# Kernel optimization log

Measured on AMD Instinct MI355X. Metric: run time of the kernel, lower is better.

Reference implementation:

```python
import jax, jax.numpy as jnp
import numpy as np

K = 20
EPS = 1e-5  # BatchNorm eps
SLOPE = 0.2  # LeakyReLU negative slope


def _lrelu(y):
    return jnp.where(y > 0, y, SLOPE * y)


def _knn_idx(x):
    # x: [B, C, N] -> idx [B, N, K] of nearest neighbors (largest of negative sq dist)
    inner = -2.0 * jnp.einsum('bcn,bcm->bnm', x, x)
    xx = jnp.sum(x * x, axis=1)  # [B, N]
    pd = -xx[:, :, None] - inner - xx[:, None, :]  # [B, N, N]
    return jax.lax.top_k(pd, K)[1]


def _graph_feature(x):
    # x: [B, C, N] -> [B, 2C, N, K] = cat(neighbor - center, center)
    idx = _knn_idx(x)
    xt = jnp.transpose(x, (0, 2, 1))  # [B, N, C]
    nb = jax.vmap(lambda f, i: f[i])(xt, idx)  # [B, N, K, C]
    ctr = xt[:, :, None, :]
    feat = jnp.concatenate([nb - ctr, jnp.broadcast_to(ctr, nb.shape)], axis=-1)
    return jnp.transpose(feat, (0, 3, 1, 2))


def _bn(y, p, ch_axis):
    g, b, m, v = p[0], p[1], p[2], p[3]
    shape = [1] * y.ndim
    shape[ch_axis] = -1
    scale = (g / jnp.sqrt(v + EPS)).reshape(shape)
    return (y - m.reshape(shape)) * scale + b.reshape(shape)


def _conv_block(x, w, bn):
    f = _graph_feature(x)  # [B, 2C_in, N, K]
    y = jnp.einsum('bcnk,oc->bonk', f, w)  # 1x1 conv, no bias
    y = _lrelu(_bn(y, bn, 1))
    return jnp.max(y, axis=-1)  # max over K neighbors -> [B, C_out, N]


def setup_inputs() -> dict:
    key = jax.random.key(0)
    ks = jax.random.split(key, 20)
    B, N = 8, 1024
    inp = {
        'x': jax.random.normal(ks[0], (B, 3, N), jnp.float32),
        'w0': jax.random.normal(ks[1], (64, 6), jnp.float32) * 0.1,
        'w1': jax.random.normal(ks[2], (64, 128), jnp.float32) * 0.1,
        'w2': jax.random.normal(ks[3], (128, 128), jnp.float32) * 0.1,
        'w3': jax.random.normal(ks[4], (256, 256), jnp.float32) * 0.1,
        'bn0': jax.random.uniform(ks[5], (4, 64), jnp.float32) + 0.1,
        'bn1': jax.random.uniform(ks[6], (4, 64), jnp.float32) + 0.1,
        'bn2': jax.random.uniform(ks[7], (4, 128), jnp.float32) + 0.1,
        'bn3': jax.random.uniform(ks[8], (4, 256), jnp.float32) + 0.1,
        'we': jax.random.normal(ks[9], (1024, 512), jnp.float32) * 0.05,
        'bne': jax.random.uniform(ks[10], (4, 1024), jnp.float32) + 0.1,
        'wf0': jax.random.normal(ks[11], (512, 2048), jnp.float32) * 0.02,
        'bnf0': jax.random.uniform(ks[12], (4, 512), jnp.float32) + 0.1,
        'wf1': jax.random.normal(ks[13], (256, 512), jnp.float32) * 0.05,
        'bnf1': jax.random.uniform(ks[14], (4, 256), jnp.float32) + 0.1,
        'wfin': jax.random.normal(ks[15], (64, 256), jnp.float32) * 0.05,
        'bfin': jax.random.normal(ks[16], (64,), jnp.float32) * 0.05,
    }
    return inp


def reference(x, w0, w1, w2, w3, bn0, bn1, bn2, bn3, we, bne, wf0, bnf0, wf1, bnf1, wfin, bfin):
    B = x.shape[0]
    x1 = _conv_block(x, w0, bn0)   # [B, 64, N]
    x2 = _conv_block(x1, w1, bn1)  # [B, 64, N]
    x3 = _conv_block(x2, w2, bn2)  # [B, 128, N]
    x4 = _conv_block(x3, w3, bn3)  # [B, 256, N]
    cat = jnp.concatenate([x1, x2, x3, x4], axis=1)  # [B, 512, N]
    e = _lrelu(_bn(jnp.einsum('bcn,oc->bon', cat, we), bne, 1))  # [B, 1024, N]
    p1 = jnp.max(e, axis=-1)
    p2 = jnp.mean(e, axis=-1)
    h = jnp.concatenate([p1, p2], axis=1)  # [B, 2048]
    h = _lrelu(_bn(h @ wf0.T, bnf0, 1))  # [B, 512]; dropout is eval-mode identity
    h = _lrelu(_bn(h @ wf1.T, bnf1, 1))  # [B, 256]
    return h @ wfin.T + bfin  # [B, 64]
```

## Files before the change

kernel.cpp:

```cpp
#include <hip/hip_runtime.h>
#include <math.h>

#define N_PTS 1024
#define BATCH 8
#define KNN 20
#define EPSB 1e-5f
#define SLOPE 0.2f

typedef __attribute__((ext_vector_type(8))) short short8;
typedef __attribute__((ext_vector_type(4))) float f32x4;
typedef unsigned short ushort_t;
typedef unsigned long long u64;

__device__ __forceinline__ float lrelu(float y) { return y > 0.f ? y : SLOPE * y; }

__device__ __forceinline__ ushort_t f2bf(float f) {
    union { float f; unsigned u; } v; v.f = f;
    unsigned r = v.u + 0x7FFF + ((v.u >> 16) & 1);
    return (ushort_t)(r >> 16);
}

__device__ __forceinline__ void wprep_one(const float* __restrict__ w, float* __restrict__ wpt,
                                          int C, int Cout, int g) {
    int M2 = 2 * Cout;
    if (g >= C * M2) return;
    int c = g / M2, m = g - c * M2;
    float v;
    if (m < Cout) v = w[(size_t)m * 2 * C + c];
    else { int o = m - Cout; v = w[(size_t)o * 2 * C + C + c] - w[(size_t)o * 2 * C + c]; }
    wpt[(size_t)c * M2 + m] = v;
}

__global__ void prep_kernel(const float* __restrict__ we, ushort_t* __restrict__ weh,
                            const float* __restrict__ w0, float* __restrict__ wpt0,
                            const float* __restrict__ w1, float* __restrict__ wpt1,
                            const float* __restrict__ w2, float* __restrict__ wpt2,
                            const float* __restrict__ w3, float* __restrict__ wpt3) {
    int bx = blockIdx.x, tid = threadIdx.x;
    if (bx < 512) {
        int g = bx * 256 + tid;
        float4 v = ((const float4*)we)[g];
        ushort4 o;
        o.x = f2bf(v.x); o.y = f2bf(v.y); o.z = f2bf(v.z); o.w = f2bf(v.w);
        ((ushort4*)weh)[g] = o;
    } else if (bx < 514) {
        wprep_one(w0, wpt0, 3, 64, (bx - 512) * 256 + tid);
    } else if (bx < 546) {
        wprep_one(w1, wpt1, 64, 64, (bx - 514) * 256 + tid);
    } else if (bx < 610) {
        wprep_one(w2, wpt2, 64, 128, (bx - 546) * 256 + tid);
    } else {
        wprep_one(w3, wpt3, 128, 256, (bx - 610) * 256 + tid);
    }
}

__global__ void __launch_bounds__(64)
xx_kernel(const float* __restrict__ x, float* __restrict__ xx, int C, int bstride) {
    int b = blockIdx.y;
    int n = blockIdx.x * 64 + threadIdx.x;
    const float* xb = x + (size_t)b * bstride + n;
    float s = 0.f;
    #pragma unroll 4
    for (int c = 0; c < C; c++) { float v = xb[(size_t)c * N_PTS]; s += v * v; }
    xx[b * N_PTS + n] = s;
}

__global__ void __launch_bounds__(256)
pdabv_kernel(const float* __restrict__ x, const float* __restrict__ wpt,
             const float* __restrict__ xx,
             float* __restrict__ pd, float* __restrict__ A, float* __restrict__ Bv,
             int C, int Cout, int bstride, int pdTiles) {
    int b = blockIdx.z;
    int nt = blockIdx.y;
    int bx = blockIdx.x;
    int tid = threadIdx.x;
    int tx = tid & 15, ty = tid >> 4;
    int n0 = nt * 128;
    __shared__ float sU0[16][128];
    __shared__ float sU1[16][128];
    const float* xb = x + (size_t)b * bstride;
    float acc[8][8] = {};
    if (bx < pdTiles) {
        int m0 = bx * 128;
        for (int c0 = 0; c0 < C; c0 += 16) {
            for (int q = 0; q < 2; q++) {
                int f = q * 256 + tid;
                int r = f >> 5, col = (f & 31) * 4;
                int c = c0 + r;
                float4 vn = {0.f, 0.f, 0.f, 0.f}, vm = {0.f, 0.f, 0.f, 0.f};
                if (c < C) {
                    vn = *(const float4*)&xb[(size_t)c * N_PTS + n0 + col];
                    vm = *(const float4*)&xb[(size_t)c * N_PTS + m0 + col];
                }
                *(float4*)&sU0[r][col] = vn;
                *(float4*)&sU1[r][col] = vm;
            }
            __syncthreads();
            for (int k = 0; k < 16; k++) {
                float4 a0 = *(const float4*)&sU0[k][ty * 4];
                float4 a1 = *(const float4*)&sU0[k][64 + ty * 4];
                float4 b0 = *(const float4*)&sU1[k][tx * 4];
                float4 b1 = *(const float4*)&sU1[k][64 + tx * 4];
                float av[8] = {a0.x, a0.y, a0.z, a0.w, a1.x, a1.y, a1.z, a1.w};
                float bw[8] = {b0.x, b0.y, b0.z, b0.w, b1.x, b1.y, b1.z, b1.w};
                for (int i = 0; i < 8; i++)
                    for (int j = 0; j < 8; j++) acc[i][j] += av[i] * bw[j];
            }
            __syncthreads();
        }
        float xm[8];
        const float* xxb = xx + b * N_PTS + m0;
        *(float4*)&xm[0] = *(const float4*)&xxb[tx * 4];
        *(float4*)&xm[4] = *(const float4*)&xxb[64 + tx * 4];
        for (int i = 0; i < 8; i++) {
            int n = n0 + (i >> 2) * 64 + ty * 4 + (i & 3);
            float* prow = pd + ((size_t)(b * N_PTS + n)) * N_PTS;
            for (int jh = 0; jh < 2; jh++) {
                float4 o;
                o.x = 2.f * acc[i][jh * 4 + 0] - xm[jh * 4 + 0];
                o.y = 2.f * acc[i][jh * 4 + 1] - xm[jh * 4 + 1];
                o.z = 2.f * acc[i][jh * 4 + 2] - xm[jh * 4 + 2];
                o.w = 2.f * acc[i][jh * 4 + 3] - xm[jh * 4 + 3];
                *(float4*)&prow[m0 + jh * 64 + tx * 4] = o;
            }
        }
    } else {
        int m0 = (bx - pdTiles) * 128;
        int M2 = 2 * Cout;
        for (int c0 = 0; c0 < C; c0 += 16) {
            for (int q = 0; q < 2; q++) {
                int f = q * 256 + tid;
                int r = f >> 5, col = (f & 31) * 4;
                int c = c0 + r;
                float4 vw = {0.f, 0.f, 0.f, 0.f}, vx = {0.f, 0.f, 0.f, 0.f};
                if (c < C) {
                    vw = *(const float4*)&wpt[(size_t)c * M2 + m0 + col];
                    vx = *(const float4*)&xb[(size_t)c * N_PTS + n0 + col];
                }
                *(float4*)&sU0[r][col] = vw;
                *(float4*)&sU1[r][col] = vx;
            }
            __syncthreads();
            for (int k = 0; k < 16; k++) {
                float4 a0 = *(const float4*)&sU0[k][ty * 4];
                float4 a1 = *(const float4*)&sU0[k][64 + ty * 4];
                float4 b0 = *(const float4*)&sU1[k][tx * 4];
                float4 b1 = *(const float4*)&sU1[k][64 + tx * 4];
                float av[8] = {a0.x, a0.y, a0.z, a0.w, a1.x, a1.y, a1.z, a1.w};
                float bw[8] = {b0.x, b0.y, b0.z, b0.w, b1.x, b1.y, b1.z, b1.w};
                for (int i = 0; i < 8; i++)
                    for (int j = 0; j < 8; j++) acc[i][j] += av[i] * bw[j];
            }
            __syncthreads();
        }
        for (int i = 0; i < 8; i++) {
            int rowm = m0 + (i >> 2) * 64 + ty * 4 + (i & 3);
            float* dst = (rowm < Cout) ? (A + ((size_t)b * Cout + rowm) * N_PTS)
                                       : (Bv + ((size_t)b * Cout + rowm - Cout) * N_PTS);
            for (int jh = 0; jh < 2; jh++) {
                float4 o;
                o.x = acc[i][jh * 4 + 0];
                o.y = acc[i][jh * 4 + 1];
                o.z = acc[i][jh * 4 + 2];
                o.w = acc[i][jh * 4 + 3];
                *(float4*)&dst[n0 + jh * 64 + tx * 4] = o;
            }
        }
    }
}

__global__ void __launch_bounds__(256)
topk_kernel(const float* __restrict__ pd, int* __restrict__ idx) {
    int wid = threadIdx.x >> 6;
    int row = blockIdx.x * 4 + wid;
    int lane = threadIdx.x & 63;
    __shared__ u64 Sk[4][64];
    const float* p = pd + (size_t)row * N_PTS;
    float v[16];
    for (int q = 0; q < 4; q++) {
        float4 t = *(const float4*)&p[lane * 16 + q * 4];
        v[q * 4 + 0] = t.x; v[q * 4 + 1] = t.y; v[q * 4 + 2] = t.z; v[q * 4 + 3] = t.w;
    }
    float lmax = v[0];
    #pragma unroll
    for (int j = 1; j < 16; j++) lmax = fmaxf(lmax, v[j]);
    float s = lmax;
    #pragma unroll
    for (int k = 2; k <= 64; k <<= 1) {
        #pragma unroll
        for (int j = k >> 1; j > 0; j >>= 1) {
            float o = __shfl_xor(s, j, 64);
            bool takeMin = (((lane & k) == 0) == ((lane & j) == 0));
            float mn = fminf(s, o), mx = fmaxf(s, o);
            s = takeMin ? mn : mx;
        }
    }
    float tp = __shfl(s, 44, 64);
    unsigned hm = 0;
    #pragma unroll
    for (int j = 0; j < 16; j++) hm |= (v[j] >= tp ? 1u : 0u) << j;
    int cnt = __popc(hm);
    int incl = cnt;
    #pragma unroll
    for (int d = 1; d < 64; d <<= 1) {
        int o = __shfl_up(incl, d, 64);
        if (lane >= d) incl += o;
    }
    int total = __shfl(incl, 63, 64);
    int pos = incl - cnt;
    if (total <= 64) {
        #pragma unroll
        for (int j = 0; j < 16; j++) {
            if (hm & (1u << j)) {
                unsigned u = __float_as_uint(v[j]);
                unsigned msk = ((unsigned)((int)u >> 31)) | 0x80000000u;
                Sk[wid][pos] = ((u64)(u ^ msk) << 32) | (unsigned)(1023 - (lane * 16 + j));
                pos++;
            }
        }
        u64 key = (lane < total) ? Sk[wid][lane] : 0ull;
        #pragma unroll
        for (int k = 2; k <= 64; k <<= 1) {
            #pragma unroll
            for (int j = k >> 1; j > 0; j >>= 1) {
                u64 o = __shfl_xor(key, j, 64);
                bool takeMin = (((lane & k) == 0) == ((lane & j) == 0));
                bool sgt = key > o;
                key = (sgt != takeMin) ? key : o;
            }
        }
        if (lane >= 44) {
            int m = 1023 - (int)(unsigned)(key & 0xFFFFFFFFu);
            idx[row * KNN + (63 - lane)] = m;
        }
    } else {
        for (int kk = 0; kk < KNN; kk++) {
            float bv = v[0]; int bj = 0;
            #pragma unroll
            for (int j = 1; j < 16; j++) if (v[j] > bv) { bv = v[j]; bj = j; }
            int bi = lane * 16 + bj;
            for (int d = 32; d > 0; d >>= 1) {
                float ov = __shfl_down(bv, d, 64);
                int oi = __shfl_down(bi, d, 64);
                if (ov > bv || (ov == bv && oi < bi)) { bv = ov; bi = oi; }
            }
            bi = __shfl(bi, 0, 64);
            if ((bi >> 4) == lane) {
                #pragma unroll
                for (int j = 0; j < 16; j++) if (j == (bi & 15)) v[j] = -INFINITY;
            }
            if (lane == 0) idx[row * KNN + kk] = bi;
        }
    }
}

__global__ void __launch_bounds__(256)
topk0_kernel(const float* __restrict__ x, int* __restrict__ idx) {
    int wid = threadIdx.x >> 6;
    int row = blockIdx.x * 4 + wid;
    int lane = threadIdx.x & 63;
    __shared__ u64 Sk[4][64];
    int b = row >> 10, n = row & 1023;
    const float* xb = x + (size_t)b * 3 * N_PTS;
    float xr0 = xb[n], xr1 = xb[N_PTS + n], xr2 = xb[2 * N_PTS + n];
    float v[16];
    for (int q = 0; q < 4; q++) {
        int base = lane * 16 + q * 4;
        float4 c0 = *(const float4*)&xb[base];
        float4 c1 = *(const float4*)&xb[N_PTS + base];
        float4 c2 = *(const float4*)&xb[2 * N_PTS + base];
        float a0[4] = {c0.x, c0.y, c0.z, c0.w};
        float a1[4] = {c1.x, c1.y, c1.z, c1.w};
        float a2[4] = {c2.x, c2.y, c2.z, c2.w};
        #pragma unroll
        for (int j = 0; j < 4; j++) {
            float d = 0.f;
            d += xr0 * a0[j]; d += xr1 * a1[j]; d += xr2 * a2[j];
            float sq = 0.f;
            sq += a0[j] * a0[j]; sq += a1[j] * a1[j]; sq += a2[j] * a2[j];
            v[q * 4 + j] = 2.f * d - sq;
        }
    }
    float lmax = v[0];
    #pragma unroll
    for (int j = 1; j < 16; j++) lmax = fmaxf(lmax, v[j]);
    float s = lmax;
    #pragma unroll
    for (int k = 2; k <= 64; k <<= 1) {
        #pragma unroll
        for (int j = k >> 1; j > 0; j >>= 1) {
            float o = __shfl_xor(s, j, 64);
            bool takeMin = (((lane & k) == 0) == ((lane & j) == 0));
            float mn = fminf(s, o), mx = fmaxf(s, o);
            s = takeMin ? mn : mx;
        }
    }
    float tp = __shfl(s, 44, 64);
    unsigned hm = 0;
    #pragma unroll
    for (int j = 0; j < 16; j++) hm |= (v[j] >= tp ? 1u : 0u) << j;
    int cnt = __popc(hm);
    int incl = cnt;
    #pragma unroll
    for (int d = 1; d < 64; d <<= 1) {
        int o = __shfl_up(incl, d, 64);
        if (lane >= d) incl += o;
    }
    int total = __shfl(incl, 63, 64);
    int pos = incl - cnt;
    if (total <= 64) {
        #pragma unroll
        for (int j = 0; j < 16; j++) {
            if (hm & (1u << j)) {
                unsigned u = __float_as_uint(v[j]);
                unsigned msk = ((unsigned)((int)u >> 31)) | 0x80000000u;
                Sk[wid][pos] = ((u64)(u ^ msk) << 32) | (unsigned)(1023 - (lane * 16 + j));
                pos++;
            }
        }
        u64 key = (lane < total) ? Sk[wid][lane] : 0ull;
        #pragma unroll
        for (int k = 2; k <= 64; k <<= 1) {
            #pragma unroll
            for (int j = k >> 1; j > 0; j >>= 1) {
                u64 o = __shfl_xor(key, j, 64);
                bool takeMin = (((lane & k) == 0) == ((lane & j) == 0));
                bool sgt = key > o;
                key = (sgt != takeMin) ? key : o;
            }
        }
        if (lane >= 44) {
            int m = 1023 - (int)(unsigned)(key & 0xFFFFFFFFu);
            idx[row * KNN + (63 - lane)] = m;
        }
    } else {
        for (int kk = 0; kk < KNN; kk++) {
            float bv = v[0]; int bj = 0;
            #pragma unroll
            for (int j = 1; j < 16; j++) if (v[j] > bv) { bv = v[j]; bj = j; }
            int bi = lane * 16 + bj;
            for (int d = 32; d > 0; d >>= 1) {
                float ov = __shfl_down(bv, d, 64);
                int oi = __shfl_down(bi, d, 64);
                if (ov > bv || (ov == bv && oi < bi)) { bv = ov; bi = oi; }
            }
            bi = __shfl(bi, 0, 64);
            if ((bi >> 4) == lane) {
                #pragma unroll
                for (int j = 0; j < 16; j++) if (j == (bi & 15)) v[j] = -INFINITY;
            }
            if (lane == 0) idx[row * KNN + kk] = bi;
        }
    }
}

__global__ void __launch_bounds__(256)
gmax_kernel(const float* __restrict__ A, const float* __restrict__ Bv,
            const int* __restrict__ idx, const float* __restrict__ bnp,
            float* __restrict__ out, int Cout, int outStrideB) {
    int b = blockIdx.z;
    int n0 = blockIdx.x * 64;
    int o0 = blockIdx.y * 4;
    int tid = threadIdx.x;
    __shared__ int sidx[64 * 21];
    __shared__ float sA[4][N_PTS];
    for (int t = tid; t < 64 * KNN; t += 256) {
        int nl = t / KNN, k = t - nl * KNN;
        sidx[nl * 21 + k] = idx[(b * N_PTS + n0) * KNN + t];
    }
    const float* Abase = A + ((size_t)b * Cout + o0) * N_PTS;
    for (int q = 0; q < 4; q++) {
        int f = q * 256 + tid;
        int r = f >> 8, c4 = (f & 255) * 4;
        *(float4*)&sA[r][c4] = *(const float4*)&Abase[(size_t)r * N_PTS + c4];
    }
    __syncthreads();
    int nl = tid & 63, ol = tid >> 6;
    float best = -INFINITY;
    #pragma unroll
    for (int k = 0; k < KNN; k++) {
        int j = sidx[nl * 21 + k];
        best = fmaxf(best, sA[ol][j]);
    }
    int o = o0 + ol;
    int n = n0 + nl;
    float pre = best + Bv[((size_t)b * Cout + o) * N_PTS + n];
    float g = bnp[o], bb = bnp[Cout + o], m = bnp[2 * Cout + o], vv = bnp[3 * Cout + o];
    float scale = g / sqrtf(vv + EPSB);
    out[(size_t)b * outStrideB + (size_t)o * N_PTS + n] = lrelu((pre - m) * scale + bb);
}

__global__ void catT_kernel(const float* __restrict__ cat, ushort_t* __restrict__ catT) {
    int b = blockIdx.z, ct = blockIdx.y, nt = blockIdx.x;
    int tid = threadIdx.x;
    __shared__ float tile[64][65];
    const float* cb = cat + (size_t)b * 512 * N_PTS;
    for (int q = 0; q < 16; q++) {
        int e = q * 256 + tid;
        int c = e >> 6, n = e & 63;
        tile[c][n] = cb[(size_t)(ct * 64 + c) * N_PTS + nt * 64 + n];
    }
    __syncthreads();
    for (int q = 0; q < 16; q++) {
        int e = q * 256 + tid;
        int n = e >> 6, c = e & 63;
        catT[((size_t)b * N_PTS + nt * 64 + n) * 512 + ct * 64 + c] = f2bf(tile[c][n]);
    }
}

__global__ void __launch_bounds__(256)
gemm6_mfma(const ushort_t* __restrict__ weh, const ushort_t* __restrict__ catT,
           const float* __restrict__ bne,
           float* __restrict__ pmax, float* __restrict__ psum) {
    int b = blockIdx.z, ot = blockIdx.y, nt = blockIdx.x;
    int tid = threadIdx.x;
    int w = tid >> 6, lane = tid & 63, q = lane >> 4, lr = lane & 15;
    int mblk = w >> 1, nblk = w & 1;
    __shared__ __align__(16) ushort_t sA[128 * 40];
    __shared__ __align__(16) ushort_t sB[128 * 40];
    __shared__ float sa[128], sc[128];
    __shared__ float redmax[128][2], redsum[128][2];
    int o0 = ot * 128, n0 = nt * 128;
    if (tid < 128) {
        int o = o0 + tid;
        float g = bne[o], bb = bne[1024 + o], m = bne[2048 + o], vv = bne[3072 + o];
        float scale = g / sqrtf(vv + EPSB);
        sa[tid] = scale; sc[tid] = bb - m * scale;
    }
    f32x4 acc[4][4] = {};
    const ushort_t* cT = catT + (size_t)b * N_PTS * 512;
    int r0 = tid >> 2, s = tid & 3;
    for (int k0 = 0; k0 < 512; k0 += 32) {
        __syncthreads();
        for (int h = 0; h < 2; h++) {
            int r = r0 + h * 64;
            *(short8*)&sA[r * 40 + s * 8] = *(const short8*)(weh + (size_t)(o0 + r) * 512 + k0 + s * 8);
            *(short8*)&sB[r * 40 + s * 8] = *(const short8*)(cT  + (size_t)(n0 + r) * 512 + k0 + s * 8);
        }
        __syncthreads();
        short8 af[4], bfr[4];
        for (int mi = 0; mi < 4; mi++)
            af[mi] = *(const short8*)&sA[(mblk * 64 + mi * 16 + lr) * 40 + q * 8];
        for (int ni = 0; ni < 4; ni++)
            bfr[ni] = *(const short8*)&sB[(nblk * 64 + ni * 16 + lr) * 40 + q * 8];
        for (int mi = 0; mi < 4; mi++)
            for (int ni = 0; ni < 4; ni++)
                acc[mi][ni] = __builtin_amdgcn_mfma_f32_16x16x32_bf16(af[mi], bfr[ni], acc[mi][ni], 0, 0, 0);
    }
    for (int mi = 0; mi < 4; mi++) {
        for (int r = 0; r < 4; r++) {
            int row = mblk * 64 + mi * 16 + q * 4 + r;
            float a = sa[row], c = sc[row];
            float mx = -INFINITY, sm = 0.f;
            for (int ni = 0; ni < 4; ni++) {
                float y = lrelu(acc[mi][ni][r] * a + c);
                mx = fmaxf(mx, y); sm += y;
            }
            for (int msk = 1; msk < 16; msk <<= 1) {
                mx = fmaxf(mx, __shfl_xor(mx, msk, 16));
                sm += __shfl_xor(sm, msk, 16);
            }
            if (lr == 0) { redmax[row][nblk] = mx; redsum[row][nblk] = sm; }
        }
    }
    __syncthreads();
    if (tid < 128) {
        float mx = fmaxf(redmax[tid][0], redmax[tid][1]);
        float sm = redsum[tid][0] + redsum[tid][1];
        int o = o0 + tid;
        pmax[((size_t)(b * 1024 + o)) * 8 + nt] = mx;
        psum[((size_t)(b * 1024 + o)) * 8 + nt] = sm;
    }
}

__global__ void pool_reduce_kernel(const float* __restrict__ pmax, const float* __restrict__ psum,
                                   float* __restrict__ h0) {
    int g = blockIdx.x * 256 + threadIdx.x;
    int b = g >> 10, o = g & 1023;
    float mx = -INFINITY, sm = 0.f;
    for (int t = 0; t < 8; t++) { mx = fmaxf(mx, pmax[g * 8 + t]); sm += psum[g * 8 + t]; }
    h0[(size_t)b * 2048 + o] = mx;
    h0[(size_t)b * 2048 + 1024 + o] = sm * (1.0f / 1024.0f);
}

__global__ void fc_kernel(const float* __restrict__ in, const float* __restrict__ w,
                          const float* __restrict__ bnp, const float* __restrict__ bias,
                          float* __restrict__ out, int Cin, int Cout, int mode) {
    int blk = blockIdx.x;
    int b = blk / Cout, o = blk % Cout;
    int lane = threadIdx.x;
    const float* inb = in + (size_t)b * Cin;
    const float* wo = w + (size_t)o * Cin;
    float acc = 0.f;
    for (int c = lane; c < Cin; c += 64) acc += inb[c] * wo[c];
    for (int s = 32; s > 0; s >>= 1) acc += __shfl_down(acc, s, 64);
    if (lane == 0) {
        float y = acc;
        if (mode == 0) {
            float g = bnp[o], bb = bnp[Cout + o], m = bnp[2 * Cout + o], vv = bnp[3 * Cout + o];
            y = lrelu((y - m) * (g / sqrtf(vv + EPSB)) + bb);
        } else {
            y += bias[o];
        }
        out[(size_t)b * Cout + o] = y;
    }
}

extern "C" void kernel_launch(void* const* d_in, const int* in_sizes, int n_in,
                              void* d_out, int out_size, void* d_ws, size_t ws_size,
                              hipStream_t stream) {
    const float* x    = (const float*)d_in[0];
    const float* w0   = (const float*)d_in[1];
    const float* w1   = (const float*)d_in[2];
    const float* w2   = (const float*)d_in[3];
    const float* w3   = (const float*)d_in[4];
    const float* bn0  = (const float*)d_in[5];
    const float* bn1  = (const float*)d_in[6];
    const float* bn2  = (const float*)d_in[7];
    const float* bn3  = (const float*)d_in[8];
    const float* we   = (const float*)d_in[9];
    const float* bne  = (const float*)d_in[10];
    const float* wf0  = (const float*)d_in[11];
    const float* bnf0 = (const float*)d_in[12];
    const float* wf1  = (const float*)d_in[13];
    const float* bnf1 = (const float*)d_in[14];
    const float* wfin = (const float*)d_in[15];
    const float* bfin = (const float*)d_in[16];

    float* ws = (float*)d_ws;
    size_t off = 0;
    float* cat  = ws + off; off += (size_t)BATCH * 512 * N_PTS;
    float* pd   = ws + off; off += (size_t)BATCH * N_PTS * N_PTS;
    float* A    = ws + off; off += (size_t)BATCH * 256 * N_PTS;
    float* Bv   = ws + off; off += (size_t)BATCH * 256 * N_PTS;
    float* xxv  = ws + off; off += (size_t)BATCH * N_PTS;
    float* pmax = ws + off; off += (size_t)BATCH * N_PTS * 8;
    float* psum = ws + off; off += (size_t)BATCH * N_PTS * 8;
    float* h0   = ws + off; off += (size_t)BATCH * 2048;
    float* h1   = ws + off; off += (size_t)BATCH * 512;
    float* h2   = ws + off; off += (size_t)BATCH * 256;
    int*   idx  = (int*)(ws + off); off += (size_t)BATCH * N_PTS * KNN;
    ushort_t* weh  = (ushort_t*)(ws + off); off += (size_t)(1024 * 512) / 2;
    ushort_t* catT = (ushort_t*)(ws + off); off += (size_t)BATCH * N_PTS * 512 / 2;
    float* wpt0 = ws + off; off += 3 * 128;
    float* wpt1 = ws + off; off += 64 * 128;
    float* wpt2 = ws + off; off += 64 * 256;
    float* wpt3 = ws + off; off += 128 * 512;

    const int CSTR = 512 * N_PTS;
    const int topkBlocks = BATCH * N_PTS / 4;

    prep_kernel<<<866, 256, 0, stream>>>(we, weh, w0, wpt0, w1, wpt1, w2, wpt2, w3, wpt3);

    pdabv_kernel<<<dim3(1, 8, BATCH), 256, 0, stream>>>(x, wpt0, xxv, pd, A, Bv, 3, 64, 3 * N_PTS, 0);
    topk0_kernel<<<topkBlocks, 256, 0, stream>>>(x, idx);
    gmax_kernel<<<dim3(16, 16, BATCH), 256, 0, stream>>>(A, Bv, idx, bn0, cat, 64, CSTR);

    xx_kernel<<<dim3(16, BATCH), 64, 0, stream>>>(cat, xxv, 64, CSTR);
    pdabv_kernel<<<dim3(9, 8, BATCH), 256, 0, stream>>>(cat, wpt1, xxv, pd, A, Bv, 64, 64, CSTR, 8);
    topk_kernel<<<topkBlocks, 256, 0, stream>>>(pd, idx);
    gmax_kernel<<<dim3(16, 16, BATCH), 256, 0, stream>>>(A, Bv, idx, bn1, cat + 64 * N_PTS, 64, CSTR);

    xx_kernel<<<dim3(16, BATCH), 64, 0, stream>>>(cat + 64 * N_PTS, xxv, 64, CSTR);
    pdabv_kernel<<<dim3(10, 8, BATCH), 256, 0, stream>>>(cat + 64 * N_PTS, wpt2, xxv, pd, A, Bv, 64, 128, CSTR, 8);
    topk_kernel<<<topkBlocks, 256, 0, stream>>>(pd, idx);
    gmax_kernel<<<dim3(16, 32, BATCH), 256, 0, stream>>>(A, Bv, idx, bn2, cat + 128 * N_PTS, 128, CSTR);

    xx_kernel<<<dim3(16, BATCH), 64, 0, stream>>>(cat + 128 * N_PTS, xxv, 128, CSTR);
    pdabv_kernel<<<dim3(12, 8, BATCH), 256, 0, stream>>>(cat + 128 * N_PTS, wpt3, xxv, pd, A, Bv, 128, 256, CSTR, 8);
    topk_kernel<<<topkBlocks, 256, 0, stream>>>(pd, idx);
    gmax_kernel<<<dim3(16, 64, BATCH), 256, 0, stream>>>(A, Bv, idx, bn3, cat + 256 * N_PTS, 256, CSTR);

    catT_kernel<<<dim3(16, 8, BATCH), 256, 0, stream>>>(cat, catT);
    gemm6_mfma<<<dim3(8, 8, BATCH), 256, 0, stream>>>(weh, catT, bne, pmax, psum);
    pool_reduce_kernel<<<32, 256, 0, stream>>>(pmax, psum, h0);

    fc_kernel<<<BATCH * 512, 64, 0, stream>>>(h0, wf0, bnf0, nullptr, h1, 2048, 512, 0);
    fc_kernel<<<BATCH * 256, 64, 0, stream>>>(h1, wf1, bnf1, nullptr, h2, 512, 256, 0);
    fc_kernel<<<BATCH * 64, 64, 0, stream>>>(h2, wfin, nullptr, bfin, (float*)d_out, 256, 64, 1);
}
```

Baseline: 351.0 us.

## Merge pdabv GEMM paths and read A operand directly from global memory

The two branches of the pd/A/B GEMM kernel are unified into one loop driven by base pointers and strides. Only the B operand is staged in shared memory, while each thread reads its A slice straight from global memory (wavefront-uniform broadcast-like loads). The inner loops are fully unrolled and launch bounds request 3 blocks per CU. This halves LDS use and staging work, but puts global-load latency inside the FMA loop and may raise register pressure under the occupancy hint.

Result: slower. 867.6 us (+147.2%).

```diff
diff --git a/kernel.cpp b/kernel.cpp
--- a/kernel.cpp
+++ b/kernel.cpp
@@ -65,7 +65,7 @@
     xx[b * N_PTS + n] = s;
 }
 
-__global__ void __launch_bounds__(256)
+__global__ void __launch_bounds__(256, 3)
 pdabv_kernel(const float* __restrict__ x, const float* __restrict__ wpt,
              const float* __restrict__ xx,
              float* __restrict__ pd, float* __restrict__ A, float* __restrict__ Bv,
@@ -76,42 +76,67 @@
     int tid = threadIdx.x;
     int tx = tid & 15, ty = tid >> 4;
     int n0 = nt * 128;
-    __shared__ float sU0[16][128];
     __shared__ float sU1[16][128];
     const float* xb = x + (size_t)b * bstride;
     float acc[8][8] = {};
-    if (bx < pdTiles) {
-        int m0 = bx * 128;
-        for (int c0 = 0; c0 < C; c0 += 16) {
-            for (int q = 0; q < 2; q++) {
-                int f = q * 256 + tid;
-                int r = f >> 5, col = (f & 31) * 4;
-                int c = c0 + r;
-                float4 vn = {0.f, 0.f, 0.f, 0.f}, vm = {0.f, 0.f, 0.f, 0.f};
-                if (c < C) {
-                    vn = *(const float4*)&xb[(size_t)c * N_PTS + n0 + col];
-                    vm = *(const float4*)&xb[(size_t)c * N_PTS + m0 + col];
-                }
-                *(float4*)&sU0[r][col] = vn;
-                *(float4*)&sU1[r][col] = vm;
-            }
-            __syncthreads();
+
+    bool isPd = bx < pdTiles;
+    int m0 = isPd ? bx * 128 : (bx - pdTiles) * 128;
+    const float* Abase = isPd ? (xb + n0) : (wpt + m0);
+    int Astride = isPd ? N_PTS : 2 * Cout;
+    const float* Bbase = isPd ? (xb + m0) : (xb + n0);
+
+    int fr = tid >> 5, fcol = (tid & 31) * 4;
+    for (int c0 = 0; c0 < C; c0 += 16) {
+        int kmax = C - c0; if (kmax > 16) kmax = 16;
+        {
+            float4 z = {0.f, 0.f, 0.f, 0.f};
+            int ca = c0 + fr, cb2 = c0 + fr + 8;
+            float4 v0 = (ca < C) ? *(const float4*)&Bbase[(size_t)ca * N_PTS + fcol] : z;
+            float4 v1 = (cb2 < C) ? *(const float4*)&Bbase[(size_t)cb2 * N_PTS + fcol] : z;
+            *(float4*)&sU1[fr][fcol] = v0;
+            *(float4*)&sU1[fr + 8][fcol] = v1;
+        }
+        __syncthreads();
+        if (kmax == 16) {
+            #pragma unroll
             for (int k = 0; k < 16; k++) {
-                float4 a0 = *(const float4*)&sU0[k][ty * 4];
-                float4 a1 = *(const float4*)&sU0[k][64 + ty * 4];
+                const float* ap = Abase + (size_t)(c0 + k) * Astride;
+                float4 a0 = *(const float4*)&ap[ty * 4];
+                float4 a1 = *(const float4*)&ap[64 + ty * 4];
                 float4 b0 = *(const float4*)&sU1[k][tx * 4];
                 float4 b1 = *(const float4*)&sU1[k][64 + tx * 4];
                 float av[8] = {a0.x, a0.y, a0.z, a0.w, a1.x, a1.y, a1.z, a1.w};
                 float bw[8] = {b0.x, b0.y, b0.z, b0.w, b1.x, b1.y, b1.z, b1.w};
+                #pragma unroll
                 for (int i = 0; i < 8; i++)
+                    #pragma unroll
                     for (int j = 0; j < 8; j++) acc[i][j] += av[i] * bw[j];
             }
-            __syncthreads();
-        }
+        } else {
+            for (int k = 0; k < kmax; k++) {
+                const float* ap = Abase + (size_t)(c0 + k) * Astride;
+                float4 a0 = *(const float4*)&ap[ty * 4];
+                float4 a1 = *(const float4*)&ap[64 + ty * 4];
+                float4 b0 = *(const float4*)&sU1[k][tx * 4];
+                float4 b1 = *(const float4*)&sU1[k][64 + tx * 4];
+                float av[8] = {a0.x, a0.y, a0.z, a0.w, a1.x, a1.y, a1.z, a1.w};
+                float bw[8] = {b0.x, b0.y, b0.z, b0.w, b1.x, b1.y, b1.z, b1.w};
+                #pragma unroll
+                for (int i = 0; i < 8; i++)
+                    #pragma unroll
+                    for (int j = 0; j < 8; j++) acc[i][j] += av[i] * bw[j];
+            }
+        }
+        __syncthreads();
+    }
+
+    if (isPd) {
         float xm[8];
         const float* xxb = xx + b * N_PTS + m0;
         *(float4*)&xm[0] = *(const float4*)&xxb[tx * 4];
         *(float4*)&xm[4] = *(const float4*)&xxb[64 + tx * 4];
+        #pragma unroll
         for (int i = 0; i < 8; i++) {
             int n = n0 + (i >> 2) * 64 + ty * 4 + (i & 3);
             float* prow = pd + ((size_t)(b * N_PTS + n)) * N_PTS;
@@ -125,34 +150,7 @@
             }
         }
     } else {
-        int m0 = (bx - pdTiles) * 128;
-        int M2 = 2 * Cout;
-        for (int c0 = 0; c0 < C; c0 += 16) {
-            for (int q = 0; q < 2; q++) {
-                int f = q * 256 + tid;
-                int r = f >> 5, col = (f & 31) * 4;
-                int c = c0 + r;
-                float4 vw = {0.f, 0.f, 0.f, 0.f}, vx = {0.f, 0.f, 0.f, 0.f};
-                if (c < C) {
-                    vw = *(const float4*)&wpt[(size_t)c * M2 + m0 + col];
-                    vx = *(const float4*)&xb[(size_t)c * N_PTS + n0 + col];
-                }
-                *(float4*)&sU0[r][col] = vw;
-                *(float4*)&sU1[r][col] = vx;
-            }
-            __syncthreads();
-            for (int k = 0; k < 16; k++) {
-                float4 a0 = *(const float4*)&sU0[k][ty * 4];
-                float4 a1 = *(const float4*)&sU0[k][64 + ty * 4];
-                float4 b0 = *(const float4*)&sU1[k][tx * 4];
-                float4 b1 = *(const float4*)&sU1[k][64 + tx * 4];
-                float av[8] = {a0.x, a0.y, a0.z, a0.w, a1.x, a1.y, a1.z, a1.w};
-                float bw[8] = {b0.x, b0.y, b0.z, b0.w, b1.x, b1.y, b1.z, b1.w};
-                for (int i = 0; i < 8; i++)
-                    for (int j = 0; j < 8; j++) acc[i][j] += av[i] * bw[j];
-            }
-            __syncthreads();
-        }
+        #pragma unroll
         for (int i = 0; i < 8; i++) {
             int rowm = m0 + (i >> 2) * 64 + ty * 4 + (i & 3);
             float* dst = (rowm < Cout) ? (A + ((size_t)b * Cout + rowm) * N_PTS)
```
